# Performance work log

Measured on AMD Instinct MI355X. Metric: run time of the kernel, lower is better.

Reference implementation:

```python
import jax, jax.numpy as jnp
import numpy as np

B, C_LOW, C_HIGH, KC, VC, H, W = 4, 512, 256, 64, 64, 64, 64


def setup_inputs() -> dict:
    key = jax.random.key(0)
    ks = jax.random.split(key, 6)
    x_low = jax.random.normal(ks[0], (B, C_LOW, H, W), dtype=jnp.float32)
    x_high = jax.random.normal(ks[1], (B, C_HIGH, H, W), dtype=jnp.float32)
    # 1x1 conv weights, fan-in scaled
    Wq = jax.random.normal(ks[2], (KC, C_HIGH), dtype=jnp.float32) / np.sqrt(C_HIGH)
    Wk = jax.random.normal(ks[3], (KC, C_LOW), dtype=jnp.float32) / np.sqrt(C_LOW)
    Wv = jax.random.normal(ks[4], (VC, C_LOW), dtype=jnp.float32) / np.sqrt(C_LOW)
    Wo = jax.random.normal(ks[5], (C_HIGH, VC), dtype=jnp.float32) / np.sqrt(VC)
    return {
        "x_low": x_low, "x_high": x_high,
        "Wq": Wq, "bq": jnp.zeros((KC,), jnp.float32),
        "Wk": Wk, "bk": jnp.zeros((KC,), jnp.float32),
        "Wv": Wv, "bv": jnp.zeros((VC,), jnp.float32),
        "Wo": Wo, "bo": jnp.zeros((C_HIGH,), jnp.float32),
    }


def reference(x_low, x_high, Wq, bq, Wk, bk, Wv, bv, Wo, bo):
    b, ch, h, w = x_high.shape
    n = h * w  # tokens per image
    # 1x1 convs == per-pixel linear maps; flatten spatial to tokens
    xh = x_high.reshape(b, ch, n)                # [B, C_high, N]
    xl = x_low.reshape(b, x_low.shape[1], n)     # [B, C_low,  N]
    q = jnp.einsum('kc,bcn->bnk', Wq, xh) + bq   # [B, N, KC]
    k = jnp.einsum('kc,bcn->bkn', Wk, xl) + bk[:, None]  # [B, KC, N]
    v = jnp.einsum('vc,bcn->bnv', Wv, xl) + bv   # [B, N, VC]
    sim = jnp.einsum('bnk,bkm->bnm', q, k)       # [B, N, N]
    attn = jax.nn.softmax(sim, axis=-1)
    ctx = jnp.einsum('bnm,bmv->bnv', attn, v)    # [B, N, VC]
    out = jnp.einsum('ov,bnv->bon', Wo, ctx) + bo[:, None]  # [B, C_high, N]
    return out.reshape(b, ch, h, w) + x_high
```

## Files before the change

kernel.cpp:

```cpp
#include <hip/hip_runtime.h>
#include <hip/hip_bf16.h>
#include <math.h>
#include <stdint.h>

#define B 4
#define CLOW 512
#define CHIGH 256
#define KC 64
#define VC 64
#define N 4096

typedef __attribute__((ext_vector_type(8))) short bf16x8;
typedef __attribute__((ext_vector_type(4))) short bf16x4;
typedef __attribute__((ext_vector_type(4))) float f32x4;

__device__ inline unsigned short f2bf(float f) {
    union { float f; uint32_t u; } v; v.f = f;
    uint32_t u = v.u;
    u += 0x7fff + ((u >> 16) & 1);
    return (unsigned short)(u >> 16);
}
__device__ inline float bf2f(unsigned short h) {
    union { uint32_t u; float f; } v; v.u = ((uint32_t)h) << 16;
    return v.f;
}
__device__ inline uint32_t packbf2(float a, float b) {
    union { __hip_bfloat16 h; unsigned short u; } ca, cb;
    ca.h = __float2bfloat16(a);
    cb.h = __float2bfloat16(b);
    return (uint32_t)ca.u | ((uint32_t)cb.u << 16);
}
__device__ inline void bfsplit(float x, short* hi, short* lo) {
    union { __hip_bfloat16 h; unsigned short u; } c, d;
    c.h = __float2bfloat16(x);
    d.h = __float2bfloat16(x - __bfloat162float(c.h));
    *hi = (short)c.u; *lo = (short)d.u;
}

#if __has_builtin(__builtin_amdgcn_exp2f)
#define EXP2(x) __builtin_amdgcn_exp2f(x)
#else
#define EXP2(x) exp2f(x)
#endif


#define CSTEP 64
__global__ __launch_bounds__(256) void proj_mfma(
    const float* __restrict__ xl, const float* __restrict__ xh,
    const float* __restrict__ Wq, const float* __restrict__ bq,
    const float* __restrict__ Wk, const float* __restrict__ bk,
    const float* __restrict__ Wv, const float* __restrict__ bv,
    unsigned short* __restrict__ Qt, unsigned short* __restrict__ Kt,
    unsigned short* __restrict__ Vt)
{
    const int proj = blockIdx.z;
    const int b    = blockIdx.y;
    const int bidx = blockIdx.x;
    const int n0   = bidx * 32;
    const int tid  = threadIdx.x;
    const int wv   = tid >> 6;
    const int lane = tid & 63;
    const int lo   = lane & 15;
    const int hi   = lane >> 4;
    const int hi8  = hi * 8;

    __shared__ unsigned short XtHi[32][72];
    __shared__ unsigned short XtLo[32][72];

    const int tS = tid & 3;
    const int t8 = tS * 8;
    const int cR = tid >> 2;

    const float* X; int C;
    if (proj == 0) { X = xh; C = CHIGH; } else { X = xl; C = CLOW; }

    float4 pf0, pf1;

    #define LOADX(C0)                                                            \
        {                                                                        \
            const float* src = X + ((size_t)b*C + (C0) + cR)*N + n0 + t8;        \
            pf0 = *(const float4*)src;                                           \
            pf1 = *(const float4*)(src + 4);                                     \
        }

    #define STAGE()                                                              \
        {                                                                        \
            const int colx = cR ^ (tS << 3);                                     \
            float vv[8] = {pf0.x, pf0.y, pf0.z, pf0.w,                           \
                           pf1.x, pf1.y, pf1.z, pf1.w};                          \
            _Pragma("unroll")                                                    \
            for (int i = 0; i < 8; ++i) {                                        \
                short h_, l_;                                                    \
                bfsplit(vv[i], &h_, &l_);                                        \
                XtHi[t8 + i][colx] = (unsigned short)h_;                         \
                XtLo[t8 + i][colx] = (unsigned short)l_;                         \
            }                                                                    \
        }

    #define WSPLITLD(WP, AH, AL)                                                 \
        {                                                                        \
            float4 w0 = *(const float4*)(WP);                                    \
            float4 w1 = *(const float4*)((WP) + 4);                              \
            float ww[8] = {w0.x,w0.y,w0.z,w0.w,w1.x,w1.y,w1.z,w1.w};             \
            _Pragma("unroll")                                                    \
            for (int i = 0; i < 8; ++i) {                                        \
                short h_, l_;                                                    \
                bfsplit(ww[i], &h_, &l_);                                        \
                AH[i] = h_; AL[i] = l_;                                          \
            }                                                                    \
        }

    const size_t kqFragOff = (size_t)((((wv*2 + (hi>>1)) & 3)*16 + lo)*8 + (hi&1)*4);

    if (proj == 0) {
        f32x4 acc[2];
        #pragma unroll
        for (int t = 0; t < 2; ++t)
            #pragma unroll
            for (int r = 0; r < 4; ++r) acc[t][r] = bq[wv*16 + hi*4 + r];

        LOADX(0)
        for (int c0 = 0; c0 < CHIGH; c0 += CSTEP) {
            STAGE()
            __syncthreads();
            if (c0 + CSTEP < CHIGH) LOADX(c0 + CSTEP)

            #pragma unroll
            for (int m = 0; m < 2; ++m) {
                bf16x8 ah, al;
                const float* wp = Wq + (size_t)(wv*16 + lo)*CHIGH + c0 + m*32 + hi8;
                WSPLITLD(wp, ah, al)
                #pragma unroll
                for (int tt = 0; tt < 2; ++tt) {
                    const int cx = (m*32 + hi8) ^ ((2*tt + (lo >> 3)) << 3);
                    bf16x8 xhv = *(const bf16x8*)&XtHi[tt*16 + lo][cx];
                    bf16x8 xlv = *(const bf16x8*)&XtLo[tt*16 + lo][cx];
                    acc[tt] = __builtin_amdgcn_mfma_f32_16x16x32_bf16(ah, xhv, acc[tt], 0, 0, 0);
                    acc[tt] = __builtin_amdgcn_mfma_f32_16x16x32_bf16(ah, xlv, acc[tt], 0, 0, 0);
                    acc[tt] = __builtin_amdgcn_mfma_f32_16x16x32_bf16(al, xhv, acc[tt], 0, 0, 0);
                }
            }
            __syncthreads();
        }
        const float qs = 1.4426950408889634f;
        #pragma unroll
        for (int t = 0; t < 2; ++t) {
            bf16x4 o;
            #pragma unroll
            for (int r = 0; r < 4; ++r) o[r] = (short)f2bf(acc[t][r] * qs);
            size_t base = (((size_t)b*256 + 2*bidx + t)*2 + (wv>>1))*512;
            *(bf16x4*)&Qt[base + kqFragOff] = o;
        }
    } else {
        f32x4 accK[2], accV[2];
        #pragma unroll
        for (int t = 0; t < 2; ++t)
            #pragma unroll
            for (int r = 0; r < 4; ++r) {
                accK[t][r] = bk[wv*16 + hi*4 + r];
                accV[t][r] = bv[wv*16 + hi*4 + r];
            }

        LOADX(0)
        for (int c0 = 0; c0 < CLOW; c0 += CSTEP) {
            STAGE()
            __syncthreads();
            if (c0 + CSTEP < CLOW) LOADX(c0 + CSTEP)

            #pragma unroll
            for (int m = 0; m < 2; ++m) {
                bf16x8 ahk, alk, ahv, alv;
                const float* wpk = Wk + (size_t)(wv*16 + lo)*CLOW + c0 + m*32 + hi8;
                const float* wpv = Wv + (size_t)(wv*16 + lo)*CLOW + c0 + m*32 + hi8;
                WSPLITLD(wpk, ahk, alk)
                WSPLITLD(wpv, ahv, alv)
                #pragma unroll
                for (int tt = 0; tt < 2; ++tt) {
                    const int cx = (m*32 + hi8) ^ ((2*tt + (lo >> 3)) << 3);
                    bf16x8 xhv = *(const bf16x8*)&XtHi[tt*16 + lo][cx];
                    bf16x8 xlv = *(const bf16x8*)&XtLo[tt*16 + lo][cx];
                    accK[tt] = __builtin_amdgcn_mfma_f32_16x16x32_bf16(ahk, xhv, accK[tt], 0, 0, 0);
                    accK[tt] = __builtin_amdgcn_mfma_f32_16x16x32_bf16(ahk, xlv, accK[tt], 0, 0, 0);
                    accK[tt] = __builtin_amdgcn_mfma_f32_16x16x32_bf16(alk, xhv, accK[tt], 0, 0, 0);
                    accV[tt] = __builtin_amdgcn_mfma_f32_16x16x32_bf16(ahv, xhv, accV[tt], 0, 0, 0);
                    accV[tt] = __builtin_amdgcn_mfma_f32_16x16x32_bf16(ahv, xlv, accV[tt], 0, 0, 0);
                    accV[tt] = __builtin_amdgcn_mfma_f32_16x16x32_bf16(alv, xhv, accV[tt], 0, 0, 0);
                }
            }
            __syncthreads();
        }

        #pragma unroll
        for (int t = 0; t < 2; ++t) {
            bf16x4 o;
            #pragma unroll
            for (int r = 0; r < 4; ++r) o[r] = (short)f2bf(accK[t][r]);
            size_t kbase = (((size_t)b*256 + 2*bidx + t)*2 + (wv>>1))*512;
            *(bf16x4*)&Kt[kbase + kqFragOff] = o;

            const int hi_f = t*2 + (lo >> 3);
            size_t vbase = ((size_t)b*128 + bidx)*2048 + (size_t)wv*512
                         + (size_t)hi_f*128 + (size_t)(lo & 7);
            #pragma unroll
            for (int r = 0; r < 4; ++r)
                Vt[vbase + (size_t)(hi*4 + r)*8] = f2bf(accV[t][r]);
        }
    }
    #undef LOADX
    #undef STAGE
    #undef WSPLITLD
}

#define WSPLIT 8
#define QT 2
__global__ __launch_bounds__(512, 4) void attn(
    const unsigned short* __restrict__ Qt,
    const unsigned short* __restrict__ Kt,
    const unsigned short* __restrict__ Vt,
    float* __restrict__ ctx)
{
    const int bid = blockIdx.x;
    const int xcd = bid & 7;
    const int b   = xcd >> 1;
    const int q0  = ((bid >> 3) * 2 + (xcd & 1)) * 32;

    const int tid  = threadIdx.x;
    const int wv   = tid >> 6;
    const int lane = tid & 63;
    const int lo   = lane & 15;
    const int hi   = lane >> 4;

    __shared__ float Olds[WSPLIT][32][68];
    __shared__ float llds[WSPLIT][32];

    const unsigned short* Kb = Kt + (size_t)b*N*KC;
    const unsigned short* Vb = Vt + (size_t)b*VC*N;
    const unsigned short* Qb = Qt + (size_t)b*N*KC;

    bf16x8 qf[2][QT];
    #pragma unroll
    for (int qt = 0; qt < QT; ++qt) {
        #pragma unroll
        for (int kt = 0; kt < 2; ++kt)
            qf[kt][qt] = *(const bf16x8*)&Qb[(((size_t)(q0>>4) + qt)*2 + kt)*512 + lane*8];
    }

    f32x4 O[4][QT] = {};
    float l_run[QT] = {};

    const int kv0   = wv * (N/WSPLIT);
    const int kvend = kv0 + (N/WSPLIT);

    for (int kv = kv0; kv < kvend; kv += 32) {
        bf16x8 ka[2][2], va[4];
        #pragma unroll
        for (int j = 0; j < 2; ++j)
            #pragma unroll
            for (int m = 0; m < 2; ++m)
                ka[j][m] = *(const bf16x8*)&Kb[(((size_t)(kv>>4) + j)*2 + m)*512 + lane*8];
        #pragma unroll
        for (int vt = 0; vt < 4; ++vt)
            va[vt] = *(const bf16x8*)&Vb[((size_t)(kv>>5))*2048 + vt*512 + lane*8];

        #pragma unroll
        for (int qt = 0; qt < QT; ++qt) {
            f32x4 st[2];
            #pragma unroll
            for (int j = 0; j < 2; ++j) {
                f32x4 z = {};
                z     = __builtin_amdgcn_mfma_f32_16x16x32_bf16(ka[j][0], qf[0][qt], z, 0, 0, 0);
                st[j] = __builtin_amdgcn_mfma_f32_16x16x32_bf16(ka[j][1], qf[1][qt], z, 0, 0, 0);
            }
            uint32_t pk[2][2];
            #pragma unroll
            for (int j = 0; j < 2; ++j) {
                float p0 = EXP2(st[j][0]);
                float p1 = EXP2(st[j][1]);
                float p2 = EXP2(st[j][2]);
                float p3 = EXP2(st[j][3]);
                l_run[qt] += (p0 + p1) + (p2 + p3);
                pk[j][0] = packbf2(p0, p1);
                pk[j][1] = packbf2(p2, p3);
            }
            union { int w[4]; bf16x8 v; } pa;
            #pragma unroll
            for (int w = 0; w < 4; ++w) {
                int src = (2*(hi & 1) + (w >> 1))*16 + lo;
                int t0 = __shfl((int)pk[0][w & 1], src);
                int t1 = __shfl((int)pk[1][w & 1], src);
                pa.w[w] = (hi < 2) ? t0 : t1;
            }
            #pragma unroll
            for (int vt = 0; vt < 4; ++vt)
                O[vt][qt] = __builtin_amdgcn_mfma_f32_16x16x32_bf16(pa.v, va[vt], O[vt][qt], 0, 0, 0);
        }
    }

    #pragma unroll
    for (int qt = 0; qt < QT; ++qt) {
        float s = l_run[qt];
        s += __shfl_xor(s, 16);
        s += __shfl_xor(s, 32);
        l_run[qt] = s;
    }

    #pragma unroll
    for (int qt = 0; qt < QT; ++qt) {
        #pragma unroll
        for (int vt = 0; vt < 4; ++vt)
            #pragma unroll
            for (int r = 0; r < 4; ++r)
                Olds[wv][qt*16 + hi*4 + r][vt*16 + lo] = O[vt][qt][r];
        if (lane < 16) llds[wv][qt*16 + lo] = l_run[qt];
    }
    __syncthreads();

    {
        const int row = tid >> 4;
        const int c4  = (tid & 15) * 4;
        float L = 0.f;
        #pragma unroll
        for (int w = 0; w < WSPLIT; ++w) L += llds[w][row];
        float4 o = {0.f, 0.f, 0.f, 0.f};
        #pragma unroll
        for (int w = 0; w < WSPLIT; ++w) {
            float4 ow = *(const float4*)&Olds[w][row][c4];
            o.x += ow.x; o.y += ow.y; o.z += ow.z; o.w += ow.w;
        }
        float rL = 1.0f / L;
        o.x *= rL; o.y *= rL; o.z *= rL; o.w *= rL;
        *(float4*)&ctx[((size_t)b*N + q0 + row)*VC + c4] = o;
    }
}

__global__ __launch_bounds__(256) void oproj_mfma(
    const float* __restrict__ ctx, const float* __restrict__ Wo,
    const float* __restrict__ bo, const float* __restrict__ xh,
    float* __restrict__ out)
{
    const int b    = blockIdx.y;
    const int n0   = blockIdx.x * 16;
    const int tid  = threadIdx.x;
    const int wv   = tid >> 6;
    const int lane = tid & 63;
    const int lo   = lane & 15;
    const int hi   = lane >> 4;
    const int hi8  = hi * 8;

    bf16x8 bh[2], bl[2];
    const float* cp = ctx + ((size_t)b*N + n0 + lo)*VC + hi8;
    #pragma unroll
    for (int j = 0; j < 2; ++j) {
        float4 c0 = *(const float4*)(cp + j*32);
        float4 c1 = *(const float4*)(cp + j*32 + 4);
        float cc[8] = {c0.x,c0.y,c0.z,c0.w,c1.x,c1.y,c1.z,c1.w};
        #pragma unroll
        for (int i = 0; i < 8; ++i) {
            short h_, l_;
            bfsplit(cc[i], &h_, &l_);
            bh[j][i] = h_;
            bl[j][i] = l_;
        }
    }
    #pragma unroll
    for (int ct = 0; ct < 4; ++ct) {
        const int chan0 = wv*64 + ct*16;
        bf16x8 ah[2], al[2];
        const float* wp = Wo + (size_t)(chan0 + lo)*VC + hi8;
        #pragma unroll
        for (int j = 0; j < 2; ++j) {
            float4 w0 = *(const float4*)(wp + j*32);
            float4 w1 = *(const float4*)(wp + j*32 + 4);
            float ww[8] = {w0.x,w0.y,w0.z,w0.w,w1.x,w1.y,w1.z,w1.w};
            #pragma unroll
            for (int i = 0; i < 8; ++i) {
                short h_, l_;
                bfsplit(ww[i], &h_, &l_);
                ah[j][i] = h_;
                al[j][i] = l_;
            }
        }
        f32x4 acc;
        #pragma unroll
        for (int r = 0; r < 4; ++r) acc[r] = bo[chan0 + hi*4 + r];
        #pragma unroll
        for (int j = 0; j < 2; ++j) {
            acc = __builtin_amdgcn_mfma_f32_16x16x32_bf16(ah[j], bh[j], acc, 0, 0, 0);
            acc = __builtin_amdgcn_mfma_f32_16x16x32_bf16(ah[j], bl[j], acc, 0, 0, 0);
            acc = __builtin_amdgcn_mfma_f32_16x16x32_bf16(al[j], bh[j], acc, 0, 0, 0);
        }
        #pragma unroll
        for (int r = 0; r < 4; ++r) {
            size_t idx = ((size_t)b*CHIGH + chan0 + hi*4 + r)*N + n0 + lo;
            out[idx] = acc[r] + xh[idx];
        }
    }
}

extern "C" void kernel_launch(void* const* d_in, const int* in_sizes, int n_in,
                              void* d_out, int out_size, void* d_ws, size_t ws_size,
                              hipStream_t stream) {
    const float* xl = (const float*)d_in[0];
    const float* xh = (const float*)d_in[1];
    const float* Wq = (const float*)d_in[2];
    const float* bq = (const float*)d_in[3];
    const float* Wk = (const float*)d_in[4];
    const float* bk = (const float*)d_in[5];
    const float* Wv = (const float*)d_in[6];
    const float* bv = (const float*)d_in[7];
    const float* Wo = (const float*)d_in[8];
    const float* bo = (const float*)d_in[9];
    float* out = (float*)d_out;

    unsigned short* Qt = (unsigned short*)d_ws;
    unsigned short* Kt = Qt + (size_t)B*N*KC;
    unsigned short* Vt = Kt + (size_t)B*N*KC;
    float*         ctxp = (float*)(Vt + (size_t)B*VC*N);

    hipLaunchKernelGGL(proj_mfma, dim3(N/32, B, 2), dim3(256), 0, stream,
                       xl, xh, Wq, bq, Wk, bk, Wv, bv, Qt, Kt, Vt);
    hipLaunchKernelGGL(attn, dim3(512), dim3(512), 0, stream,
                       Qt, Kt, Vt, ctxp);
    hipLaunchKernelGGL(oproj_mfma, dim3(N/16, B), dim3(256), 0, stream,
                       ctxp, Wo, bo, xh, out);
}
```

Measured before the change: 70.77 us.

## Fuse output projection and residual into attention kernel epilogue

The separate oproj kernel is removed. The attention kernel now writes the normalized context tile to LDS and applies the Wo projection, bias and residual add directly with split-bf16 MFMAs. This drops the global ctx write and read round trip and one kernel launch. In exchange each attention block does extra epilogue work and reloads Wo from global memory, and only 512 blocks run the projection where the old kernel used 1024.

Result: faster. 62.90 us (-11.1%).

```diff
diff --git a/kernel.cpp b/kernel.cpp
--- a/kernel.cpp
+++ b/kernel.cpp
@@ -19,10 +19,6 @@
     uint32_t u = v.u;
     u += 0x7fff + ((u >> 16) & 1);
     return (unsigned short)(u >> 16);
-}
-__device__ inline float bf2f(unsigned short h) {
-    union { uint32_t u; float f; } v; v.u = ((uint32_t)h) << 16;
-    return v.f;
 }
 __device__ inline uint32_t packbf2(float a, float b) {
     union { __hip_bfloat16 h; unsigned short u; } ca, cb;
@@ -213,11 +209,12 @@
 
 #define WSPLIT 8
 #define QT 2
-__global__ __launch_bounds__(512, 4) void attn(
+__global__ __launch_bounds__(512, 4) void attn_oproj(
     const unsigned short* __restrict__ Qt,
     const unsigned short* __restrict__ Kt,
     const unsigned short* __restrict__ Vt,
-    float* __restrict__ ctx)
+    const float* __restrict__ Wo, const float* __restrict__ bo,
+    const float* __restrict__ xh, float* __restrict__ out)
 {
     const int bid = blockIdx.x;
     const int xcd = bid & 7;
@@ -229,6 +226,7 @@
     const int lane = tid & 63;
     const int lo   = lane & 15;
     const int hi   = lane >> 4;
+    const int hi8  = hi * 8;
 
     __shared__ float Olds[WSPLIT][32][68];
     __shared__ float llds[WSPLIT][32];
@@ -329,70 +327,64 @@
         }
         float rL = 1.0f / L;
         o.x *= rL; o.y *= rL; o.z *= rL; o.w *= rL;
-        *(float4*)&ctx[((size_t)b*N + q0 + row)*VC + c4] = o;
-    }
-}
-
-__global__ __launch_bounds__(256) void oproj_mfma(
-    const float* __restrict__ ctx, const float* __restrict__ Wo,
-    const float* __restrict__ bo, const float* __restrict__ xh,
-    float* __restrict__ out)
-{
-    const int b    = blockIdx.y;
-    const int n0   = blockIdx.x * 16;
-    const int tid  = threadIdx.x;
-    const int wv   = tid >> 6;
-    const int lane = tid & 63;
-    const int lo   = lane & 15;
-    const int hi   = lane >> 4;
-    const int hi8  = hi * 8;
-
-    bf16x8 bh[2], bl[2];
-    const float* cp = ctx + ((size_t)b*N + n0 + lo)*VC + hi8;
-    #pragma unroll
-    for (int j = 0; j < 2; ++j) {
-        float4 c0 = *(const float4*)(cp + j*32);
-        float4 c1 = *(const float4*)(cp + j*32 + 4);
-        float cc[8] = {c0.x,c0.y,c0.z,c0.w,c1.x,c1.y,c1.z,c1.w};
-        #pragma unroll
-        for (int i = 0; i < 8; ++i) {
-            short h_, l_;
-            bfsplit(cc[i], &h_, &l_);
-            bh[j][i] = h_;
-            bl[j][i] = l_;
-        }
-    }
-    #pragma unroll
-    for (int ct = 0; ct < 4; ++ct) {
-        const int chan0 = wv*64 + ct*16;
-        bf16x8 ah[2], al[2];
-        const float* wp = Wo + (size_t)(chan0 + lo)*VC + hi8;
-        #pragma unroll
-        for (int j = 0; j < 2; ++j) {
-            float4 w0 = *(const float4*)(wp + j*32);
-            float4 w1 = *(const float4*)(wp + j*32 + 4);
-            float ww[8] = {w0.x,w0.y,w0.z,w0.w,w1.x,w1.y,w1.z,w1.w};
-            #pragma unroll
-            for (int i = 0; i < 8; ++i) {
-                short h_, l_;
-                bfsplit(ww[i], &h_, &l_);
-                ah[j][i] = h_;
-                al[j][i] = l_;
-            }
-        }
-        f32x4 acc;
-        #pragma unroll
-        for (int r = 0; r < 4; ++r) acc[r] = bo[chan0 + hi*4 + r];
-        #pragma unroll
-        for (int j = 0; j < 2; ++j) {
-            acc = __builtin_amdgcn_mfma_f32_16x16x32_bf16(ah[j], bh[j], acc, 0, 0, 0);
-            acc = __builtin_amdgcn_mfma_f32_16x16x32_bf16(ah[j], bl[j], acc, 0, 0, 0);
-            acc = __builtin_amdgcn_mfma_f32_16x16x32_bf16(al[j], bh[j], acc, 0, 0, 0);
-        }
-        #pragma unroll
-        for (int r = 0; r < 4; ++r) {
-            size_t idx = ((size_t)b*CHIGH + chan0 + hi*4 + r)*N + n0 + lo;
-            out[idx] = acc[r] + xh[idx];
+        *(float4*)&Olds[0][row][c4] = o;
+    }
+    __syncthreads();
+
+    {
+        bf16x8 bh[2][2], bl[2][2];
+        #pragma unroll
+        for (int tt = 0; tt < 2; ++tt) {
+            #pragma unroll
+            for (int j = 0; j < 2; ++j) {
+                const float* cp = &Olds[0][tt*16 + lo][j*32 + hi8];
+                float4 c0 = *(const float4*)(cp);
+                float4 c1 = *(const float4*)(cp + 4);
+                float cc[8] = {c0.x,c0.y,c0.z,c0.w,c1.x,c1.y,c1.z,c1.w};
+                #pragma unroll
+                for (int i = 0; i < 8; ++i) {
+                    short h_, l_;
+                    bfsplit(cc[i], &h_, &l_);
+                    bh[tt][j][i] = h_;
+                    bl[tt][j][i] = l_;
+                }
+            }
+        }
+        #pragma unroll
+        for (int ct = 0; ct < 2; ++ct) {
+            const int chan0 = wv*32 + ct*16;
+            bf16x8 ah[2], al[2];
+            #pragma unroll
+            for (int j = 0; j < 2; ++j) {
+                const float* wp = Wo + (size_t)(chan0 + lo)*VC + j*32 + hi8;
+                float4 w0 = *(const float4*)(wp);
+                float4 w1 = *(const float4*)(wp + 4);
+                float ww[8] = {w0.x,w0.y,w0.z,w0.w,w1.x,w1.y,w1.z,w1.w};
+                #pragma unroll
+                for (int i = 0; i < 8; ++i) {
+                    short h_, l_;
+                    bfsplit(ww[i], &h_, &l_);
+                    ah[j][i] = h_;
+                    al[j][i] = l_;
+                }
+            }
+            #pragma unroll
+            for (int tt = 0; tt < 2; ++tt) {
+                f32x4 acc;
+                #pragma unroll
+                for (int r = 0; r < 4; ++r) acc[r] = bo[chan0 + hi*4 + r];
+                #pragma unroll
+                for (int j = 0; j < 2; ++j) {
+                    acc = __builtin_amdgcn_mfma_f32_16x16x32_bf16(ah[j], bh[tt][j], acc, 0, 0, 0);
+                    acc = __builtin_amdgcn_mfma_f32_16x16x32_bf16(ah[j], bl[tt][j], acc, 0, 0, 0);
+                    acc = __builtin_amdgcn_mfma_f32_16x16x32_bf16(al[j], bh[tt][j], acc, 0, 0, 0);
+                }
+                #pragma unroll
+                for (int r = 0; r < 4; ++r) {
+                    size_t idx = ((size_t)b*CHIGH + chan0 + hi*4 + r)*N + q0 + tt*16 + lo;
+                    out[idx] = acc[r] + xh[idx];
+                }
+            }
         }
     }
 }
@@ -415,12 +407,9 @@
     unsigned short* Qt = (unsigned short*)d_ws;
     unsigned short* Kt = Qt + (size_t)B*N*KC;
     unsigned short* Vt = Kt + (size_t)B*N*KC;
-    float*         ctxp = (float*)(Vt + (size_t)B*VC*N);
 
     hipLaunchKernelGGL(proj_mfma, dim3(N/32, B, 2), dim3(256), 0, stream,
                        xl, xh, Wq, bq, Wk, bk, Wv, bv, Qt, Kt, Vt);
-    hipLaunchKernelGGL(attn, dim3(512), dim3(512), 0, stream,
-                       Qt, Kt, Vt, ctxp);
-    hipLaunchKernelGGL(oproj_mfma, dim3(N/16, B), dim3(256), 0, stream,
-                       ctxp, Wo, bo, xh, out);
-}
+    hipLaunchKernelGGL(attn_oproj, dim3(512), dim3(512), 0, stream,
+                       Qt, Kt, Vt, Wo, bo, xh, out);
+}
```
